# Kernel tuning notes

Measured on AMD Instinct MI355X. Metric: run time of the kernel, lower is better.

Reference implementation:

```python
import jax, jax.numpy as jnp
import numpy as np

N_ITERS = 5

def setup_inputs() -> dict:
    key = jax.random.key(0)
    k_in, k_ind, k_w = jax.random.split(key, 3)
    inputs = jax.random.normal(k_in, (2, 256, 256, 1), dtype=jnp.float32)
    # indices must be valid for spatial dims [256,256] (iter 1) and [217,721] (iters 2-5)
    ind1 = jax.random.randint(k_ind, (367, 217, 721, 2), 0, 217, dtype=jnp.int32)
    w1 = jax.random.uniform(k_w, (367, 217, 721, 1, 1), dtype=jnp.float32)
    lambda1 = jnp.asarray(0.1, dtype=jnp.float32)
    return {"inputs": inputs, "ind1": ind1, "w1": w1, "lambda1": lambda1}


def reference(inputs, ind1, w1, lambda1):
    # inputs: [B,H,W,C]; ind1: [367,217,721,2]; w1: [367,217,721,1,1]; lambda1: scalar
    i0 = ind1[..., 0]  # [367,217,721] -> indexes dim0 of [H,W,C,B]
    i1 = ind1[..., 1]  # [367,217,721] -> indexes dim1
    y = inputs
    for _ in range(N_ITERS):
        yt = jnp.transpose(y, (1, 2, 3, 0))          # [H,W,C,B]
        gathered = yt[i0, i1]                        # [367,217,721,C,B] (gather_nd)
        y = jnp.sum(gathered * w1, axis=0)           # [217,721,C,B]
        y = jnp.transpose(y, (3, 0, 1, 2))           # [B,217,721,C]
        y = lambda1 * y
    return y
```

## Files before the change

### kernel.cpp

```cpp
#include <hip/hip_runtime.h>
#include <hip/hip_fp16.h>
#include <stdint.h>

#define K_    367
#define P_    217
#define Q_    721
#define QC    217
#define CPQ   (QC*QC)
#define CPQV  47092
#define TPQ   109368
#define YSTR  47104
#define PQ_   (P_*Q_)
#define TOT   ((long long)K_*PQ_)
#define NC    ((long long)K_*CPQ)
#define NVC   (CPQV/4)
#define NVT   (TPQ/4)
#define NPAD  (3*K_)
#define LDSH  47092

__device__ __forceinline__ uint32_t encode_entry(int i0, int i1, float wv) {
    uint32_t idx2 = ((uint32_t)(i0 * QC + i1)) << 1;
    uint32_t hb = (uint32_t)__half_as_ushort(__float2half(wv));
    return idx2 | (hb << 17);
}

#define GATHER(X, ACC) { uint32_t x_ = (X); \
    float g_ = __half2float(*(const __half*)((const char*)ylds + (x_ & 0x1FFFEu))); \
    float w_ = __half2float(__ushort_as_half((unsigned short)(x_ >> 17))); \
    ACC = fmaf(w_, g_, ACC); }

#define FILL_LDS() { \
    const float4* s4_ = (const float4*)yplane; \
    __half2* d2_ = (__half2*)ylds; \
    for (int i_ = threadIdx.x; i_ < LDSH / 4; i_ += 1024) { \
        float4 v_ = s4_[i_]; \
        d2_[2 * i_]     = __floats2half2_rn(v_.x, v_.y); \
        d2_[2 * i_ + 1] = __floats2half2_rn(v_.z, v_.w); \
    } }

__global__ __launch_bounds__(256) void pack_corner(
    const int2* __restrict__ ind, const float* __restrict__ w,
    const float* __restrict__ inp,
    uint32_t* __restrict__ cornerS, float* __restrict__ ybase,
    float* __restrict__ out)
{
    long long id = (long long)blockIdx.x * 256 + threadIdx.x;
    if (id < NC) {
        uint32_t o = (uint32_t)id;
        uint32_t k = o / (uint32_t)CPQ;
        uint32_t r = o - k * (uint32_t)CPQ;
        uint32_t p = r / (uint32_t)QC;
        uint32_t q = r - p * (uint32_t)QC;
        long long raw = (long long)k * PQ_ + p * Q_ + q;
        unsigned long long rr =
            __builtin_nontemporal_load((const unsigned long long*)(ind + raw));
        float wv = __builtin_nontemporal_load(w + raw);
        cornerS[k * (uint32_t)CPQV + r] =
            encode_entry((int)(uint32_t)(rr & 0xFFFFFFFFull),
                         (int)(uint32_t)(rr >> 32), wv);
        return;
    }
    long long e = id - NC;
    if (e < CPQ) {
        int o = (int)e;
        int p = o / QC, q = o - p * QC;
        ybase[o]        = inp[p * 256 + q];
        ybase[YSTR + o] = inp[65536 + p * 256 + q];
        return;
    }
    e -= CPQ;
    if (e < NPAD) {
        int k = (int)(e / 3);
        cornerS[(long long)k * CPQV + CPQ + (int)(e - (long long)k * 3)] = 0u;
        return;
    }
    e -= NPAD;
    if (e < 8 * YSTR) {
        ybase[2 * YSTR + e] = 0.f;
        return;
    }
    e -= 8 * YSTR;
    if (e < 2 * PQ_) out[e] = 0.f;
}

__global__ __launch_bounds__(1024) void iter_corner(
    const uint32_t* __restrict__ cs, const float* __restrict__ yin,
    float* __restrict__ yout, const float* __restrict__ lam_p, int KS)
{
    __shared__ __half ylds[LDSH];
    const int bz = blockIdx.z;
    const float* __restrict__ yplane = yin + (size_t)bz * YSTR;
    FILL_LDS();
    __syncthreads();
    const int gx = (NVC + 1023) / 1024;
    const int nunits = gx * KS;
    const float ls = *lam_p;
    const uint4* cs4 = (const uint4*)cs;
    for (int unit = blockIdx.x; unit < nunits; unit += gridDim.x) {
        int ob = unit % gx, kc = unit / gx;
        int ov = ob * 1024 + threadIdx.x;
        if (ov >= NVC) continue;
        int k0 = kc * K_ / KS, k1 = (kc + 1) * K_ / KS;
        float a0 = 0.f, a1 = 0.f, a2 = 0.f, a3 = 0.f;
        const uint4* pp = cs4 + (long long)k0 * NVC + ov;
        #pragma unroll 8
        for (int k = k0; k < k1; ++k, pp += NVC) {
            uint4 v = *pp;
            GATHER(v.x, a0); GATHER(v.y, a1); GATHER(v.z, a2); GATHER(v.w, a3);
        }
        float* op = yout + (size_t)bz * YSTR + 4 * ov;
        atomicAdd(op + 0, a0 * ls);
        atomicAdd(op + 1, a1 * ls);
        atomicAdd(op + 2, a2 * ls);
        atomicAdd(op + 3, a3 * ls);
    }
}

__global__ __launch_bounds__(1024) void iter_final(
    const uint32_t* __restrict__ cs,
    const int2* __restrict__ ind, const float* __restrict__ w,
    const float* __restrict__ yin, float* __restrict__ out,
    const float* __restrict__ lam_p, int KS)
{
    __shared__ __half ylds[LDSH];
    const int bz = blockIdx.z;
    const float* __restrict__ yplane = yin + (size_t)bz * YSTR;
    FILL_LDS();
    __syncthreads();
    const int NV = NVC + NVT;
    const int gx = (NV + 1023) / 1024;
    const int nunits = gx * KS;
    const float ls = *lam_p;
    for (int unit = blockIdx.x; unit < nunits; unit += gridDim.x) {
        int ob = unit % gx, kc = unit / gx;
        int ov = ob * 1024 + threadIdx.x;
        if (ov >= NV) continue;
        int k0 = kc * K_ / KS, k1 = (kc + 1) * K_ / KS;
        float a0 = 0.f, a1 = 0.f, a2 = 0.f, a3 = 0.f;
        if (ov < NVC) {
            const uint4* pp = (const uint4*)cs + (long long)k0 * NVC + ov;
            #pragma unroll 8
            for (int k = k0; k < k1; ++k, pp += NVC) {
                uint4 v = *pp;
                GATHER(v.x, a0); GATHER(v.y, a1); GATHER(v.z, a2); GATHER(v.w, a3);
            }
            float acc[4] = {a0, a1, a2, a3};
            int o0 = 4 * ov;
            #pragma unroll
            for (int j = 0; j < 4; ++j) {
                int oo = o0 + j;
                if (oo >= CPQ) continue;
                int p = oo / QC;
                int pos = p * Q_ + (oo - p * QC);
                atomicAdd(&out[(size_t)bz * PQ_ + pos], acc[j] * ls);
            }
        } else {
            int lv = ov - NVC;
            int t = 4 * lv;
            int p = t / 504;
            int q2 = t - p * 504;
            long long rawb = (long long)p * Q_ + QC + q2;
            const int2*  ip = ind + (long long)k0 * PQ_ + rawb;
            const float* wp = w   + (long long)k0 * PQ_ + rawb;
            #pragma unroll 4
            for (int k = k0; k < k1; ++k, ip += PQ_, wp += PQ_) {
                uint4 ia, ib; float4 wv;
                __builtin_memcpy(&ia, ip, 16);
                __builtin_memcpy(&ib, ip + 2, 16);
                __builtin_memcpy(&wv, wp, 16);
                a0 = fmaf(wv.x, __half2float(ylds[ia.x * QC + ia.y]), a0);
                a1 = fmaf(wv.y, __half2float(ylds[ia.z * QC + ia.w]), a1);
                a2 = fmaf(wv.z, __half2float(ylds[ib.x * QC + ib.y]), a2);
                a3 = fmaf(wv.w, __half2float(ylds[ib.z * QC + ib.w]), a3);
            }
            float acc[4] = {a0, a1, a2, a3};
            #pragma unroll
            for (int j = 0; j < 4; ++j) {
                int pos = p * Q_ + QC + q2 + j;
                atomicAdd(&out[(size_t)bz * PQ_ + pos], acc[j] * ls);
            }
        }
    }
}

extern "C" void kernel_launch(void* const* d_in, const int* in_sizes, int n_in,
                              void* d_out, int out_size, void* d_ws, size_t ws_size,
                              hipStream_t stream)
{
    const float* inp = (const float*)d_in[0];
    const int2*  ind = (const int2*)d_in[1];
    const float* w1  = (const float*)d_in[2];
    const float* lam = (const float*)d_in[3];
    float* out = (float*)d_out;

    size_t cbytes = ((((size_t)K_ * CPQV) * 4) + 255) & ~(size_t)255;
    size_t YB = (size_t)(2 * YSTR) * sizeof(float);
    if (ws_size < cbytes + 5 * YB) return;

    uint8_t* ws = (uint8_t*)d_ws;
    uint32_t* cornerS = (uint32_t*)ws;
    float* ybase = (float*)(ws + cbytes);
    float* y[5];
    for (int i = 0; i < 5; ++i) y[i] = ybase + (size_t)i * (2 * YSTR);

    long long nwork = NC + CPQ + NPAD + 8LL * YSTR + 2LL * PQ_;
    unsigned nb = (unsigned)((nwork + 255) / 256);
    pack_corner<<<dim3(nb), 256, 0, stream>>>(ind, w1, inp, cornerS, ybase, out);

    dim3 gC(120, 1, 2), gF(117, 1, 2);
    for (int it = 0; it < 4; ++it)
        iter_corner<<<gC, 1024, 0, stream>>>(cornerS, y[it], y[it + 1], lam, 10);
    iter_final<<<gF, 1024, 0, stream>>>(cornerS, ind, w1, y[4], out, lam, 6);
}
```

Baseline: 349.8 us.

## Drop packed corner buffer and gather directly from raw indices and weights

Removes the pre-pass that encoded the corner sub-block of indices and weights into compact 4-byte entries (fp16 weight plus flat index). Each of the four iterations now reads the raw int2 indices and fp32 weights directly. The final step is split into separate corner and tail kernels, each with a fixed grid mapping. This saves the packing pass and its workspace, but every iteration now moves about three times as many bytes per entry, and the loads lose 16-byte alignment because of the 721-wide row stride.

```diff
diff --git a/kernel.cpp b/kernel.cpp
--- a/kernel.cpp
+++ b/kernel.cpp
@@ -7,27 +7,11 @@
 #define Q_    721
 #define QC    217
 #define CPQ   (QC*QC)
-#define CPQV  47092
-#define TPQ   109368
 #define YSTR  47104
 #define PQ_   (P_*Q_)
-#define TOT   ((long long)K_*PQ_)
-#define NC    ((long long)K_*CPQ)
-#define NVC   (CPQV/4)
-#define NVT   (TPQ/4)
-#define NPAD  (3*K_)
 #define LDSH  47092
-
-__device__ __forceinline__ uint32_t encode_entry(int i0, int i1, float wv) {
-    uint32_t idx2 = ((uint32_t)(i0 * QC + i1)) << 1;
-    uint32_t hb = (uint32_t)__half_as_ushort(__float2half(wv));
-    return idx2 | (hb << 17);
-}
-
-#define GATHER(X, ACC) { uint32_t x_ = (X); \
-    float g_ = __half2float(*(const __half*)((const char*)ylds + (x_ & 0x1FFFEu))); \
-    float w_ = __half2float(__ushort_as_half((unsigned short)(x_ >> 17))); \
-    ACC = fmaf(w_, g_, ACC); }
+#define NU4C  (217*55)
+#define NVT   (109368/4)
 
 #define FILL_LDS() { \
     const float4* s4_ = (const float4*)yplane; \
@@ -38,86 +22,63 @@
         d2_[2 * i_ + 1] = __floats2half2_rn(v_.z, v_.w); \
     } }
 
-__global__ __launch_bounds__(256) void pack_corner(
-    const int2* __restrict__ ind, const float* __restrict__ w,
-    const float* __restrict__ inp,
-    uint32_t* __restrict__ cornerS, float* __restrict__ ybase,
+__global__ __launch_bounds__(256) void setup_all(
+    const float* __restrict__ inp, float* __restrict__ ybase,
     float* __restrict__ out)
 {
     long long id = (long long)blockIdx.x * 256 + threadIdx.x;
-    if (id < NC) {
-        uint32_t o = (uint32_t)id;
-        uint32_t k = o / (uint32_t)CPQ;
-        uint32_t r = o - k * (uint32_t)CPQ;
-        uint32_t p = r / (uint32_t)QC;
-        uint32_t q = r - p * (uint32_t)QC;
-        long long raw = (long long)k * PQ_ + p * Q_ + q;
-        unsigned long long rr =
-            __builtin_nontemporal_load((const unsigned long long*)(ind + raw));
-        float wv = __builtin_nontemporal_load(w + raw);
-        cornerS[k * (uint32_t)CPQV + r] =
-            encode_entry((int)(uint32_t)(rr & 0xFFFFFFFFull),
-                         (int)(uint32_t)(rr >> 32), wv);
-        return;
-    }
-    long long e = id - NC;
-    if (e < CPQ) {
-        int o = (int)e;
+    if (id < CPQ) {
+        int o = (int)id;
         int p = o / QC, q = o - p * QC;
         ybase[o]        = inp[p * 256 + q];
         ybase[YSTR + o] = inp[65536 + p * 256 + q];
         return;
     }
-    e -= CPQ;
-    if (e < NPAD) {
-        int k = (int)(e / 3);
-        cornerS[(long long)k * CPQV + CPQ + (int)(e - (long long)k * 3)] = 0u;
-        return;
-    }
-    e -= NPAD;
-    if (e < 8 * YSTR) {
-        ybase[2 * YSTR + e] = 0.f;
-        return;
-    }
+    long long e = id - CPQ;
+    if (e < 8 * YSTR) { ybase[2 * YSTR + e] = 0.f; return; }
     e -= 8 * YSTR;
     if (e < 2 * PQ_) out[e] = 0.f;
 }
 
-__global__ __launch_bounds__(1024) void iter_corner(
-    const uint32_t* __restrict__ cs, const float* __restrict__ yin,
-    float* __restrict__ yout, const float* __restrict__ lam_p, int KS)
+__global__ __launch_bounds__(1024) void iter_raw(
+    const int2* __restrict__ ind, const float* __restrict__ w,
+    const float* __restrict__ yin, float* __restrict__ yout,
+    const float* __restrict__ lam_p, int KS)
 {
     __shared__ __half ylds[LDSH];
     const int bz = blockIdx.z;
     const float* __restrict__ yplane = yin + (size_t)bz * YSTR;
     FILL_LDS();
     __syncthreads();
-    const int gx = (NVC + 1023) / 1024;
-    const int nunits = gx * KS;
     const float ls = *lam_p;
-    const uint4* cs4 = (const uint4*)cs;
-    for (int unit = blockIdx.x; unit < nunits; unit += gridDim.x) {
-        int ob = unit % gx, kc = unit / gx;
-        int ov = ob * 1024 + threadIdx.x;
-        if (ov >= NVC) continue;
-        int k0 = kc * K_ / KS, k1 = (kc + 1) * K_ / KS;
-        float a0 = 0.f, a1 = 0.f, a2 = 0.f, a3 = 0.f;
-        const uint4* pp = cs4 + (long long)k0 * NVC + ov;
-        #pragma unroll 8
-        for (int k = k0; k < k1; ++k, pp += NVC) {
-            uint4 v = *pp;
-            GATHER(v.x, a0); GATHER(v.y, a1); GATHER(v.z, a2); GATHER(v.w, a3);
-        }
-        float* op = yout + (size_t)bz * YSTR + 4 * ov;
-        atomicAdd(op + 0, a0 * ls);
-        atomicAdd(op + 1, a1 * ls);
-        atomicAdd(op + 2, a2 * ls);
-        atomicAdd(op + 3, a3 * ls);
+    int ob = blockIdx.x % 12, kc = blockIdx.x / 12;
+    int k0 = kc * K_ / KS, k1 = (kc + 1) * K_ / KS;
+    int ov = ob * 1024 + threadIdx.x;
+    if (ov >= NU4C) return;
+    int p = ov / 55, u = ov - p * 55;
+    int q0 = 4 * u;
+    long long rawb = (long long)p * Q_ + q0;
+    const int2*  ip = ind + (long long)k0 * PQ_ + rawb;
+    const float* wp = w   + (long long)k0 * PQ_ + rawb;
+    float a0 = 0.f, a1 = 0.f, a2 = 0.f, a3 = 0.f;
+    #pragma unroll 4
+    for (int k = k0; k < k1; ++k, ip += PQ_, wp += PQ_) {
+        int4 ia, ib; float4 wv;
+        __builtin_memcpy(&ia, ip, 16);
+        __builtin_memcpy(&ib, ip + 2, 16);
+        __builtin_memcpy(&wv, wp, 16);
+        a0 = fmaf(wv.x, __half2float(ylds[ia.x * QC + ia.y]), a0);
+        a1 = fmaf(wv.y, __half2float(ylds[ia.z * QC + ia.w]), a1);
+        a2 = fmaf(wv.z, __half2float(ylds[ib.x * QC + ib.y]), a2);
+        a3 = fmaf(wv.w, __half2float(ylds[ib.z * QC + ib.w]), a3);
     }
+    float acc[4] = {a0, a1, a2, a3};
+    int nv = QC - q0; if (nv > 4) nv = 4;
+    float* op = yout + (size_t)bz * YSTR + p * QC + q0;
+    for (int j = 0; j < nv; ++j) atomicAdd(op + j, acc[j] * ls);
 }
 
-__global__ __launch_bounds__(1024) void iter_final(
-    const uint32_t* __restrict__ cs,
+__global__ __launch_bounds__(1024) void final_corner(
     const int2* __restrict__ ind, const float* __restrict__ w,
     const float* __restrict__ yin, float* __restrict__ out,
     const float* __restrict__ lam_p, int KS)
@@ -127,59 +88,73 @@
     const float* __restrict__ yplane = yin + (size_t)bz * YSTR;
     FILL_LDS();
     __syncthreads();
-    const int NV = NVC + NVT;
-    const int gx = (NV + 1023) / 1024;
-    const int nunits = gx * KS;
     const float ls = *lam_p;
-    for (int unit = blockIdx.x; unit < nunits; unit += gridDim.x) {
-        int ob = unit % gx, kc = unit / gx;
+    int ob = blockIdx.x % 12, kc = blockIdx.x / 12;
+    int k0 = kc * K_ / KS, k1 = (kc + 1) * K_ / KS;
+    int ov = ob * 1024 + threadIdx.x;
+    if (ov >= NU4C) return;
+    int p = ov / 55, u = ov - p * 55;
+    int q0 = 4 * u;
+    long long rawb = (long long)p * Q_ + q0;
+    const int2*  ip = ind + (long long)k0 * PQ_ + rawb;
+    const float* wp = w   + (long long)k0 * PQ_ + rawb;
+    float a0 = 0.f, a1 = 0.f, a2 = 0.f, a3 = 0.f;
+    #pragma unroll 4
+    for (int k = k0; k < k1; ++k, ip += PQ_, wp += PQ_) {
+        int4 ia, ib; float4 wv;
+        __builtin_memcpy(&ia, ip, 16);
+        __builtin_memcpy(&ib, ip + 2, 16);
+        __builtin_memcpy(&wv, wp, 16);
+        a0 = fmaf(wv.x, __half2float(ylds[ia.x * QC + ia.y]), a0);
+        a1 = fmaf(wv.y, __half2float(ylds[ia.z * QC + ia.w]), a1);
+        a2 = fmaf(wv.z, __half2float(ylds[ib.x * QC + ib.y]), a2);
+        a3 = fmaf(wv.w, __half2float(ylds[ib.z * QC + ib.w]), a3);
+    }
+    float acc[4] = {a0, a1, a2, a3};
+    int nv = QC - q0; if (nv > 4) nv = 4;
+    float* op = out + (size_t)bz * PQ_ + (long long)p * Q_ + q0;
+    for (int j = 0; j < nv; ++j) atomicAdd(op + j, acc[j] * ls);
+}
+
+__global__ __launch_bounds__(1024) void final_tail(
+    const int2* __restrict__ ind, const float* __restrict__ w,
+    const float* __restrict__ yin, float* __restrict__ out,
+    const float* __restrict__ lam_p, int KS)
+{
+    __shared__ __half ylds[LDSH];
+    const int bz = blockIdx.z;
+    const float* __restrict__ yplane = yin + (size_t)bz * YSTR;
+    FILL_LDS();
+    __syncthreads();
+    const float ls = *lam_p;
+    for (int uu = 0; uu < 3; ++uu) {
+        int unit = blockIdx.x + uu * 126;
+        int ob = unit % 27, kc = unit / 27;
+        int k0 = kc * K_ / KS, k1 = (kc + 1) * K_ / KS;
         int ov = ob * 1024 + threadIdx.x;
-        if (ov >= NV) continue;
-        int k0 = kc * K_ / KS, k1 = (kc + 1) * K_ / KS;
+        if (ov >= NVT) continue;
+        int t = 4 * ov;
+        int p = t / 504;
+        int q2 = t - p * 504;
+        long long rawb = (long long)p * Q_ + QC + q2;
+        const int2*  ip = ind + (long long)k0 * PQ_ + rawb;
+        const float* wp = w   + (long long)k0 * PQ_ + rawb;
         float a0 = 0.f, a1 = 0.f, a2 = 0.f, a3 = 0.f;
-        if (ov < NVC) {
-            const uint4* pp = (const uint4*)cs + (long long)k0 * NVC + ov;
-            #pragma unroll 8
-            for (int k = k0; k < k1; ++k, pp += NVC) {
-                uint4 v = *pp;
-                GATHER(v.x, a0); GATHER(v.y, a1); GATHER(v.z, a2); GATHER(v.w, a3);
-            }
-            float acc[4] = {a0, a1, a2, a3};
-            int o0 = 4 * ov;
-            #pragma unroll
-            for (int j = 0; j < 4; ++j) {
-                int oo = o0 + j;
-                if (oo >= CPQ) continue;
-                int p = oo / QC;
-                int pos = p * Q_ + (oo - p * QC);
-                atomicAdd(&out[(size_t)bz * PQ_ + pos], acc[j] * ls);
-            }
-        } else {
-            int lv = ov - NVC;
-            int t = 4 * lv;
-            int p = t / 504;
-            int q2 = t - p * 504;
-            long long rawb = (long long)p * Q_ + QC + q2;
-            const int2*  ip = ind + (long long)k0 * PQ_ + rawb;
-            const float* wp = w   + (long long)k0 * PQ_ + rawb;
-            #pragma unroll 4
-            for (int k = k0; k < k1; ++k, ip += PQ_, wp += PQ_) {
-                uint4 ia, ib; float4 wv;
-                __builtin_memcpy(&ia, ip, 16);
-                __builtin_memcpy(&ib, ip + 2, 16);
-                __builtin_memcpy(&wv, wp, 16);
-                a0 = fmaf(wv.x, __half2float(ylds[ia.x * QC + ia.y]), a0);
-                a1 = fmaf(wv.y, __half2float(ylds[ia.z * QC + ia.w]), a1);
-                a2 = fmaf(wv.z, __half2float(ylds[ib.x * QC + ib.y]), a2);
-                a3 = fmaf(wv.w, __half2float(ylds[ib.z * QC + ib.w]), a3);
-            }
-            float acc[4] = {a0, a1, a2, a3};
-            #pragma unroll
-            for (int j = 0; j < 4; ++j) {
-                int pos = p * Q_ + QC + q2 + j;
-                atomicAdd(&out[(size_t)bz * PQ_ + pos], acc[j] * ls);
-            }
+        #pragma unroll 4
+        for (int k = k0; k < k1; ++k, ip += PQ_, wp += PQ_) {
+            int4 ia, ib; float4 wv;
+            __builtin_memcpy(&ia, ip, 16);
+            __builtin_memcpy(&ib, ip + 2, 16);
+            __builtin_memcpy(&wv, wp, 16);
+            a0 = fmaf(wv.x, __half2float(ylds[ia.x * QC + ia.y]), a0);
+            a1 = fmaf(wv.y, __half2float(ylds[ia.z * QC + ia.w]), a1);
+            a2 = fmaf(wv.z, __half2float(ylds[ib.x * QC + ib.y]), a2);
+            a3 = fmaf(wv.w, __half2float(ylds[ib.z * QC + ib.w]), a3);
         }
+        float acc[4] = {a0, a1, a2, a3};
+        float* op = out + (size_t)bz * PQ_ + (long long)p * Q_ + QC + q2;
+        #pragma unroll
+        for (int j = 0; j < 4; ++j) atomicAdd(op + j, acc[j] * ls);
     }
 }
 
@@ -193,22 +168,20 @@
     const float* lam = (const float*)d_in[3];
     float* out = (float*)d_out;
 
-    size_t cbytes = ((((size_t)K_ * CPQV) * 4) + 255) & ~(size_t)255;
     size_t YB = (size_t)(2 * YSTR) * sizeof(float);
-    if (ws_size < cbytes + 5 * YB) return;
+    if (ws_size < 5 * YB) return;
 
-    uint8_t* ws = (uint8_t*)d_ws;
-    uint32_t* cornerS = (uint32_t*)ws;
-    float* ybase = (float*)(ws + cbytes);
+    float* ybase = (float*)d_ws;
     float* y[5];
     for (int i = 0; i < 5; ++i) y[i] = ybase + (size_t)i * (2 * YSTR);
 
-    long long nwork = NC + CPQ + NPAD + 8LL * YSTR + 2LL * PQ_;
+    long long nwork = CPQ + 8LL * YSTR + 2LL * PQ_;
     unsigned nb = (unsigned)((nwork + 255) / 256);
-    pack_corner<<<dim3(nb), 256, 0, stream>>>(ind, w1, inp, cornerS, ybase, out);
+    setup_all<<<dim3(nb), 256, 0, stream>>>(inp, ybase, out);
 
-    dim3 gC(120, 1, 2), gF(117, 1, 2);
+    dim3 gC(120, 1, 2), gT(126, 1, 2);
     for (int it = 0; it < 4; ++it)
-        iter_corner<<<gC, 1024, 0, stream>>>(cornerS, y[it], y[it + 1], lam, 10);
-    iter_final<<<gF, 1024, 0, stream>>>(cornerS, ind, w1, y[4], out, lam, 6);
+        iter_raw<<<gC, 1024, 0, stream>>>(ind, w1, y[it], y[it + 1], lam, 10);
+    final_corner<<<gC, 1024, 0, stream>>>(ind, w1, y[4], out, lam, 10);
+    final_tail<<<gT, 1024, 0, stream>>>(ind, w1, y[4], out, lam, 14);
 }
```

After: 435.0 us. 24.4% more time.
